# Optimization experiments

Hardware: AMD Instinct MI355X
Metric: run time of the kernel (lower is better)

The kernel has to match this reference:

```python
import jax, jax.numpy as jnp
import numpy as np
from jax import lax

B, T, H, W, C = 1, 8, 32, 32, 512


def _rmsnorm(x, gamma):
    # x / (||x||_2 + 1e-8) * sqrt(C) * gamma  (matches FlaxHunyuanVideo15RMSNorm)
    n = x / (jnp.linalg.norm(x, axis=-1, keepdims=True) + 1e-8)
    return n * (x.shape[-1] ** 0.5) * gamma


def _conv3d(x, w, b):
    # x: [B,T,H,W,Cin], w: [kt,kh,kw,Cin,Cout] (DHWIO), VALID padding
    y = lax.conv_general_dilated(x, w, (1, 1, 1), 'VALID',
                                 dimension_numbers=('NDHWC', 'DHWIO', 'NDHWC'))
    return y + b


def _causal_conv3d(x, w, b):
    # replicate pad: time (2,0) causal, spatial (1,1) each side, then valid 3x3x3 conv
    xp = jnp.pad(x, [(0, 0), (2, 0), (1, 1), (1, 1), (0, 0)], mode='edge')
    return _conv3d(xp, w, b)


def _conv1x1(x, w, b):
    # w: [1,1,1,Cin,Cout]
    return jnp.einsum('bthwc,cd->bthwd', x, w[0, 0, 0]) + b


def _resnet(x, g1, w1, b1, g2, w2, b2):
    h = jax.nn.silu(_rmsnorm(x, g1))
    h = _causal_conv3d(h, w1, b1)
    h = jax.nn.silu(_rmsnorm(h, g2))
    h = _causal_conv3d(h, w2, b2)
    return h + x


def _attn(x, g, qw, qb, kw, kb, vw, vb, pw, pb):
    identity = x
    xn = _rmsnorm(x, g)
    b, t, h, w, c = xn.shape
    n_hw = h * w
    s = t * n_hw
    q = _conv1x1(xn, qw, qb).reshape(b, s, c)
    k = _conv1x1(xn, kw, kb).reshape(b, s, c)
    v = _conv1x1(xn, vw, vb).reshape(b, s, c)
    # block-causal frame mask: query at frame f attends to keys with frame <= f
    fid = jnp.arange(s) // n_hw
    mask = jnp.where(fid[None, :] <= fid[:, None], 0.0, -jnp.inf).astype(q.dtype)
    scale = 1.0 / jnp.sqrt(jnp.asarray(c, q.dtype))
    scores = jnp.einsum('bqc,bkc->bqk', q, k) * scale + mask  # [B,S,S]
    attn = jax.nn.softmax(scores, axis=-1)
    o = jnp.einsum('bqk,bkc->bqc', attn, v).reshape(b, t, h, w, c)
    o = _conv1x1(o, pw, pb)
    return o + identity


def _forward(x, r1_g1, r1_w1, r1_b1, r1_g2, r1_w2, r1_b2,
             at_g, q_w, q_b, k_w, k_b, v_w, v_b, p_w, p_b,
             r2_g1, r2_w1, r2_b1, r2_g2, r2_w2, r2_b2):
    h = _resnet(x, r1_g1, r1_w1, r1_b1, r1_g2, r1_w2, r1_b2)
    h = _attn(h, at_g, q_w, q_b, k_w, k_b, v_w, v_b, p_w, p_b)
    h = _resnet(h, r2_g1, r2_w1, r2_b1, r2_g2, r2_w2, r2_b2)
    return h


def setup_inputs() -> dict:
    key = jax.random.key(0)
    ks = jax.random.split(key, 10)
    w3 = lambda k: jax.random.normal(k, (3, 3, 3, C, C), jnp.float32) * 0.02
    w1 = lambda k: jax.random.normal(k, (1, 1, 1, C, C), jnp.float32) * 0.02
    zc = jnp.zeros((C,), jnp.float32)
    oc = jnp.ones((C,), jnp.float32)
    return dict(
        x=jax.random.normal(ks[0], (B, T, H, W, C), jnp.float32),
        r1_g1=oc, r1_w1=w3(ks[1]), r1_b1=zc,
        r1_g2=oc, r1_w2=w3(ks[2]), r1_b2=zc,
        at_g=oc,
        q_w=w1(ks[3]), q_b=zc,
        k_w=w1(ks[4]), k_b=zc,
        v_w=w1(ks[5]), v_b=zc,
        p_w=w1(ks[6]), p_b=zc,
        r2_g1=oc, r2_w1=w3(ks[7]), r2_b1=zc,
        r2_g2=oc, r2_w2=w3(ks[8]), r2_b2=zc,
    )


def reference(x, r1_g1, r1_w1, r1_b1, r1_g2, r1_w2, r1_b2,
              at_g, q_w, q_b, k_w, k_b, v_w, v_b, p_w, p_b,
              r2_g1, r2_w1, r2_b1, r2_g2, r2_w2, r2_b2):
    return _forward(x, r1_g1, r1_w1, r1_b1, r1_g2, r1_w2, r1_b2,
                    at_g, q_w, q_b, k_w, k_b, v_w, v_b, p_w, p_b,
                    r2_g1, r2_w1, r2_b1, r2_g2, r2_w2, r2_b2)
```

## Files before the change

kernel.cpp:

```cpp
#include <hip/hip_runtime.h>
#include <cstdint>
#include <cstddef>

typedef __attribute__((ext_vector_type(4))) float floatx4;
typedef __attribute__((ext_vector_type(8))) short short8;

__device__ __forceinline__ short f2bf(float x) {
  union { float f; unsigned u; } c; c.f = x;
  unsigned r = (c.u + 0x7FFFu + ((c.u >> 16) & 1u)) >> 16;
  return (short)r;
}

__device__ __forceinline__ float bf2f(short x) {
  union { unsigned u; float f; } c; c.u = ((unsigned)(unsigned short)x) << 16;
  return c.f;
}

__device__ __forceinline__ floatx4 mfma16(short8 a, short8 b, floatx4 c) {
  return __builtin_amdgcn_mfma_f32_16x16x32_bf16(a, b, c, 0, 0, 0);
}

template <typename T>
__device__ __forceinline__ void gl_lds16(const T* g, T* l) {
  __builtin_amdgcn_global_load_lds(
      (__attribute__((address_space(1))) void*)g,
      (__attribute__((address_space(3))) void*)l, 16, 0, 0);
}

template <bool PAD, bool SILU>
__global__ __launch_bounds__(256) void norm_kernel(const float* __restrict__ src,
                                                   const float* __restrict__ gamma,
                                                   short* __restrict__ dst) {
  const int tid = threadIdx.x;
  const int wv = tid >> 6, lane = tid & 63;
  const int id = blockIdx.x * 4 + wv;
  int srow;
  if (PAD) {
    int tp = id / 1156, rem = id - tp * 1156;
    int hp = rem / 34, wp = rem - hp * 34;
    int t = tp - 2; t = t < 0 ? 0 : t;
    int h = hp - 1; h = h < 0 ? 0 : (h > 31 ? 31 : h);
    int w = wp - 1; w = w < 0 ? 0 : (w > 31 ? 31 : w);
    srow = (t << 10) + (h << 5) + w;
  } else {
    srow = id;
  }
  const float* sp = src + (size_t)srow * 512 + lane * 8;
  float4 v0 = *(const float4*)sp;
  float4 v1 = *(const float4*)(sp + 4);
  float a[8] = {v0.x, v0.y, v0.z, v0.w, v1.x, v1.y, v1.z, v1.w};
  float ss = 0.f;
#pragma unroll
  for (int i = 0; i < 8; ++i) ss += a[i] * a[i];
#pragma unroll
  for (int off = 32; off > 0; off >>= 1) ss += __shfl_xor(ss, off);
  const float scale = 22.627416997969522f / (sqrtf(ss) + 1e-8f);
  const float* gp = gamma + lane * 8;
  float4 g0 = *(const float4*)gp;
  float4 g1 = *(const float4*)(gp + 4);
  float g[8] = {g0.x, g0.y, g0.z, g0.w, g1.x, g1.y, g1.z, g1.w};
  short8 ov;
#pragma unroll
  for (int i = 0; i < 8; ++i) {
    float y = a[i] * scale * g[i];
    if (SILU) y = y / (1.f + __expf(-y));
    ov[i] = f2bf(y);
  }
  *(short8*)(dst + (size_t)id * 512 + lane * 8) = ov;
}

__global__ __launch_bounds__(256) void combine_norm(const float* __restrict__ P0,
                                                    const float* __restrict__ P1,
                                                    const float* __restrict__ bias,
                                                    const float* __restrict__ gamma,
                                                    short* __restrict__ dst) {
  const int tid = threadIdx.x;
  const int wv = tid >> 6, lane = tid & 63;
  const int id = blockIdx.x * 4 + wv;
  int tp = id / 1156, rem = id - tp * 1156;
  int hp = rem / 34, wp = rem - hp * 34;
  int t = tp - 2; t = t < 0 ? 0 : t;
  int h = hp - 1; h = h < 0 ? 0 : (h > 31 ? 31 : h);
  int w = wp - 1; w = w < 0 ? 0 : (w > 31 ? 31 : w);
  const int srow = (t << 10) + (h << 5) + w;
  const float* sp0 = P0 + (size_t)srow * 512 + lane * 8;
  const float* sp1 = P1 + (size_t)srow * 512 + lane * 8;
  float4 a0 = *(const float4*)sp0, a1 = *(const float4*)(sp0 + 4);
  float4 b0 = *(const float4*)sp1, b1 = *(const float4*)(sp1 + 4);
  float4 z0 = *(const float4*)(bias + lane * 8), z1 = *(const float4*)(bias + lane * 8 + 4);
  float a[8] = {a0.x + b0.x + z0.x, a0.y + b0.y + z0.y, a0.z + b0.z + z0.z, a0.w + b0.w + z0.w,
                a1.x + b1.x + z1.x, a1.y + b1.y + z1.y, a1.z + b1.z + z1.z, a1.w + b1.w + z1.w};
  float ss = 0.f;
#pragma unroll
  for (int i = 0; i < 8; ++i) ss += a[i] * a[i];
#pragma unroll
  for (int off = 32; off > 0; off >>= 1) ss += __shfl_xor(ss, off);
  const float scale = 22.627416997969522f / (sqrtf(ss) + 1e-8f);
  float4 g0 = *(const float4*)(gamma + lane * 8), g1 = *(const float4*)(gamma + lane * 8 + 4);
  float g[8] = {g0.x, g0.y, g0.z, g0.w, g1.x, g1.y, g1.z, g1.w};
  short8 ov;
#pragma unroll
  for (int i = 0; i < 8; ++i) {
    float y = a[i] * scale * g[i];
    y = y / (1.f + __expf(-y));
    ov[i] = f2bf(y);
  }
  *(short8*)(dst + (size_t)id * 512 + lane * 8) = ov;
}

__global__ __launch_bounds__(256) void transpose_w(const float* __restrict__ src,
                                                   short* __restrict__ dst, int R, int C) {
  __shared__ float t[32][33];
  const int tx = threadIdx.x & 31, ty = threadIdx.x >> 5;
  const int r0 = (int)blockIdx.x << 5, c0 = (int)blockIdx.y << 5;
#pragma unroll
  for (int i = 0; i < 4; ++i)
    t[ty + i * 8][tx] = src[(size_t)(r0 + ty + i * 8) * C + c0 + tx];
  __syncthreads();
#pragma unroll
  for (int i = 0; i < 4; ++i)
    dst[(size_t)(c0 + ty + i * 8) * R + r0 + tx] = f2bf(t[tx][ty + i * 8]);
}

__global__ __launch_bounds__(256) void conv_gemm_sp(const short* __restrict__ Xp,
                                                    const short* __restrict__ WT,
                                                    float* __restrict__ P0,
                                                    float* __restrict__ P1) {
  __shared__ __attribute__((aligned(16))) short Alds[2][4096];
  __shared__ __attribute__((aligned(16))) short Blds[2][4096];
  const int tid = threadIdx.x;
  const int wv = tid >> 6, lane = tid & 63;
  const int m0 = (int)blockIdx.x << 7, n0 = (int)blockIdx.y << 7;
  const int z = blockIdx.z;
  float* __restrict__ dst = z ? P1 : P0;

  int aoff[2], boff[2];
#pragma unroll
  for (int j = 0; j < 2; ++j) {
    const int chunk = wv * 2 + j;
    const int m = m0 + chunk * 16 + (lane >> 2);
    const int t = m >> 10, h = (m >> 5) & 31, w = m & 31;
    aoff[j] = (t * 1156 + h * 34 + w) * 512 + (lane & 3) * 8;
    const int n = n0 + chunk * 16 + (lane >> 2);
    boff[j] = n * 13824 + (lane & 3) * 8;
  }
  const int wm = (wv & 1) << 6, wn = (wv >> 1) << 6;
  floatx4 acc[4][4];
#pragma unroll
  for (int i = 0; i < 4; ++i)
#pragma unroll
    for (int j = 0; j < 4; ++j) acc[i][j] = 0.f;

  const int la = (lane & 15) * 32 + (lane >> 4) * 8;
  const int k0 = z * 216, k1 = k0 + 216;

  auto stage = [&](int kk, int buf) {
    const int tap = kk >> 4;
    const int cin0 = (kk & 15) << 5;
    const int dt = tap / 9;
    const int r9 = tap - dt * 9;
    const int dh = r9 / 3;
    const int dw = r9 - dh * 3;
    const int tapoff = (dt * 1156 + dh * 34 + dw) * 512 + cin0;
#pragma unroll
    for (int j = 0; j < 2; ++j) {
      const int chunk = wv * 2 + j;
      gl_lds16(Xp + aoff[j] + tapoff, &Alds[buf][chunk * 512]);
      gl_lds16(WT + boff[j] + (kk << 5), &Blds[buf][chunk * 512]);
    }
  };

  stage(k0, 0);
  for (int kk = k0; kk < k1; ++kk) {
    const int cur = (kk - k0) & 1;
    __syncthreads();
    if (kk + 1 < k1) stage(kk + 1, cur ^ 1);
    short8 af[4], bf[4];
#pragma unroll
    for (int i = 0; i < 4; ++i) af[i] = *(const short8*)&Alds[cur][(wm + i * 16) * 32 + la];
#pragma unroll
    for (int j = 0; j < 4; ++j) bf[j] = *(const short8*)&Blds[cur][(wn + j * 16) * 32 + la];
#pragma unroll
    for (int i = 0; i < 4; ++i)
#pragma unroll
      for (int j = 0; j < 4; ++j) acc[i][j] = mfma16(af[i], bf[j], acc[i][j]);
  }

  const int rbase = m0 + wm + (lane >> 4) * 4;
#pragma unroll
  for (int i = 0; i < 4; ++i) {
    const int row = rbase + i * 16;
#pragma unroll
    for (int j = 0; j < 4; ++j) {
      const int col = n0 + wn + j * 16 + (lane & 15);
#pragma unroll
      for (int r = 0; r < 4; ++r)
        dst[(size_t)(row + r) * 512 + col] = acc[i][j][r];
    }
  }
}

template <bool HAS_RES>
__global__ __launch_bounds__(256) void conv_combine(const float* __restrict__ P0,
                                                    const float* __restrict__ P1,
                                                    const float* __restrict__ bias,
                                                    const float* __restrict__ res,
                                                    float* __restrict__ out) {
  const size_t i = ((size_t)blockIdx.x * 256 + threadIdx.x) * 4;
  float4 a = *(const float4*)(P0 + i);
  float4 b = *(const float4*)(P1 + i);
  float4 bz = *(const float4*)(bias + (int)(i & 511));
  float4 r;
  r.x = a.x + b.x + bz.x;
  r.y = a.y + b.y + bz.y;
  r.z = a.z + b.z + bz.z;
  r.w = a.w + b.w + bz.w;
  if (HAS_RES) {
    float4 rs = *(const float4*)(res + i);
    r.x += rs.x; r.y += rs.y; r.z += rs.z; r.w += rs.w;
  }
  *(float4*)(out + i) = r;
}

template <int EPI>
__global__ __launch_bounds__(256) void gemm_bt(const short* __restrict__ A,
                                               const short* __restrict__ BT, int kdim,
                                               const float* __restrict__ b0,
                                               const float* __restrict__ b1,
                                               const float* __restrict__ b2,
                                               short* __restrict__ o0,
                                               short* __restrict__ o1,
                                               short* __restrict__ o2,
                                               float* oF, const float* res) {
  __shared__ __attribute__((aligned(16))) short Alds[2][4096];
  __shared__ __attribute__((aligned(16))) short Blds[2][4096];
  const int tid = threadIdx.x;
  const int wv = tid >> 6, lane = tid & 63;
  const int m0 = (int)blockIdx.x << 7, n0 = (int)blockIdx.y << 7;
  int aoff[2], boff[2];
#pragma unroll
  for (int j = 0; j < 2; ++j) {
    const int chunk = wv * 2 + j;
    aoff[j] = (m0 + chunk * 16 + (lane >> 2)) * kdim + (lane & 3) * 8;
    boff[j] = (n0 + chunk * 16 + (lane >> 2)) * kdim + (lane & 3) * 8;
  }
  const int wm = (wv & 1) << 6, wn = (wv >> 1) << 6;
  floatx4 acc[4][4];
#pragma unroll
  for (int i = 0; i < 4; ++i)
#pragma unroll
    for (int j = 0; j < 4; ++j) acc[i][j] = 0.f;
  const int la = (lane & 15) * 32 + (lane >> 4) * 8;
  const int kiters = kdim >> 5;

  auto stage = [&](int kk, int buf) {
#pragma unroll
    for (int j = 0; j < 2; ++j) {
      const int chunk = wv * 2 + j;
      gl_lds16(A + aoff[j] + (kk << 5), &Alds[buf][chunk * 512]);
      gl_lds16(BT + boff[j] + (kk << 5), &Blds[buf][chunk * 512]);
    }
  };

  stage(0, 0);
  for (int kk = 0; kk < kiters; ++kk) {
    const int cur = kk & 1;
    __syncthreads();
    if (kk + 1 < kiters) stage(kk + 1, cur ^ 1);
    short8 af[4], bf[4];
#pragma unroll
    for (int i = 0; i < 4; ++i) af[i] = *(const short8*)&Alds[cur][(wm + i * 16) * 32 + la];
#pragma unroll
    for (int j = 0; j < 4; ++j) bf[j] = *(const short8*)&Blds[cur][(wn + j * 16) * 32 + la];
#pragma unroll
    for (int i = 0; i < 4; ++i)
#pragma unroll
      for (int j = 0; j < 4; ++j) acc[i][j] = mfma16(af[i], bf[j], acc[i][j]);
  }

  const int rbase = m0 + wm + (lane >> 4) * 4;
#pragma unroll
  for (int i = 0; i < 4; ++i) {
    const int row = rbase + i * 16;
#pragma unroll
    for (int j = 0; j < 4; ++j) {
      const int col = n0 + wn + j * 16 + (lane & 15);
      if (EPI == 0) {
        const int sel = col >> 9;
        const int c = col & 511;
        const float* bp = sel == 0 ? b0 : (sel == 1 ? b1 : b2);
        const float bz = bp[c];
#pragma unroll
        for (int r = 0; r < 4; ++r) {
          const int rr = row + r;
          const short v = f2bf(acc[i][j][r] + bz);
          if (sel == 0) {
            o0[(size_t)rr * 512 + c] = v;
          } else if (sel == 1) {
            o1[(size_t)(rr >> 5) * 16384 + ((c >> 5) << 10) + (((c >> 3) & 3) << 8) +
               ((rr & 31) << 3) + (c & 7)] = v;
          } else {
            o2[(size_t)(rr >> 5) * 16384 + (((rr >> 3) & 3) << 12) + (c << 3) + (rr & 7)] = v;
          }
        }
      } else {
        const float bz = b0[col];
#pragma unroll
        for (int r = 0; r < 4; ++r) {
          const size_t idx = (size_t)(row + r) * 512 + col;
          oF[idx] = acc[i][j][r] + bz + res[idx];
        }
      }
    }
  }
}

__global__ __launch_bounds__(512, 2) void attn_partial(const short* __restrict__ Q,
                                                       const short* __restrict__ Ksw,
                                                       const short* __restrict__ Vsw,
                                                       short* __restrict__ OpA,
                                                       short* __restrict__ OpB,
                                                       float* __restrict__ Lp) {
  __shared__ __attribute__((aligned(16))) short Kl[2][16384];
  __shared__ __attribute__((aligned(16))) short Vl[2][16384];
  __shared__ __attribute__((aligned(16))) short Plds[8][512];
  const int tid = threadIdx.x;
  const int wv = tid >> 6, lane = tid & 63;
  const int cl = lane & 15, quad = lane >> 4;
  const int bid = (int)blockIdx.x;
  const int u = ((bid >> 5) << 3) | (bid & 7);
  const int w4 = (bid >> 3) & 3;
  const int y = u >> 1;
  const int qb = ((u & 1) << 2) | w4;
  int f = 0;
  while ((f + 1) * (f + 2) / 2 <= y) ++f;
  const int chunk = y - f * (f + 1) / 2;
  const int pidx = y * 8 + qb;
  const int q0 = (f << 10) + (qb << 7);

  short8 qf[16];
  {
    const short* qp = Q + (size_t)(q0 + wv * 16 + cl) * 512 + quad * 8;
#pragma unroll
    for (int kc = 0; kc < 16; ++kc) qf[kc] = *(const short8*)(qp + kc * 32);
  }
  floatx4 o[32];
#pragma unroll
  for (int i = 0; i < 32; ++i) o[i] = 0.f;
  float lr[4] = {0.f, 0.f, 0.f, 0.f};
  const float c1 = 0.063758716f;
  const int swr = ((cl >> 1) & 3) << 3;

  auto stage = [&](int kt, int buf) {
    const size_t tb = (size_t)((chunk << 5) + kt) * 16384;
    const short* kg = Ksw + tb + (wv << 11);
    const short* vg = Vsw + tb + (wv << 11);
    short* kl = &Kl[buf][wv << 11];
    short* vl = &Vl[buf][wv << 11];
#pragma unroll
    for (int i = 0; i < 4; ++i) {
      gl_lds16(kg + (i << 9) + lane * 8, kl + (i << 9));
      gl_lds16(vg + (i << 9) + lane * 8, vl + (i << 9));
    }
  };

  stage(0, 0);
  for (int kt = 0; kt < 32; ++kt) {
    const int cur = kt & 1;
    __syncthreads();
    if (kt + 1 < 32) stage(kt + 1, cur ^ 1);

    const short* klb = &Kl[cur][quad * 256 + cl * 8];
    floatx4 s0 = 0.f, s1 = 0.f;
#pragma unroll
    for (int kc = 0; kc < 16; ++kc) {
      short8 k0 = *(const short8*)(klb + kc * 1024);
      short8 k1 = *(const short8*)(klb + kc * 1024 + 128);
      s0 = mfma16(qf[kc], k0, s0);
      s1 = mfma16(qf[kc], k1, s1);
    }

#pragma unroll
    for (int r = 0; r < 4; ++r) {
      const float p0 = exp2f(s0[r] * c1), p1 = exp2f(s1[r] * c1);
      float ps = p0 + p1;
      ps += __shfl_xor(ps, 1);
      ps += __shfl_xor(ps, 2);
      ps += __shfl_xor(ps, 4);
      ps += __shfl_xor(ps, 8);
      lr[r] += ps;
      const int qlr = quad * 4 + r;
      const int sw = ((qlr >> 1) & 3) << 3;
      const int oi = qlr * 32 + (cl ^ sw);
      Plds[wv][oi] = f2bf(p0);
      Plds[wv][oi ^ 16] = f2bf(p1);
    }
    const short8 pf = *(const short8*)&Plds[wv][cl * 32 + ((quad << 3) ^ swr)];
    const short* vlb = &Vl[cur][quad * 4096 + cl * 8];
#pragma unroll
    for (int cn = 0; cn < 32; ++cn) {
      const short8 vf = *(const short8*)(vlb + cn * 128);
      o[cn] = mfma16(pf, vf, o[cn]);
    }
  }

  short* base = pidx < 108 ? OpA + (size_t)pidx * 65536 : OpB + (size_t)(pidx - 108) * 65536;
  const int lrow0 = wv * 16 + quad * 4;
#pragma unroll
  for (int cn = 0; cn < 32; ++cn) {
    const int col = cn * 16 + cl;
#pragma unroll
    for (int r = 0; r < 4; ++r)
      base[(size_t)(lrow0 + r) * 512 + col] = f2bf(o[cn][r]);
  }
  if (cl == 0) {
#pragma unroll
    for (int r = 0; r < 4; ++r) Lp[pidx * 128 + lrow0 + r] = lr[r];
  }
}

__global__ __launch_bounds__(256) void attn_combine(const short* __restrict__ OpA,
                                                    const short* __restrict__ OpB,
                                                    const float* __restrict__ Lp,
                                                    short* __restrict__ O) {
  const int tid = threadIdx.x;
  const int wv = tid >> 6, lane = tid & 63;
  const int row = (int)blockIdx.x * 4 + wv;
  const int f = row >> 10, n = f + 1;
  const int qb = (row >> 7) & 7, lrow = row & 127;
  const int tri = f * (f + 1) / 2;
  float den = 0.f, acc[8];
#pragma unroll
  for (int i = 0; i < 8; ++i) acc[i] = 0.f;
#pragma unroll
  for (int ch = 0; ch < 8; ++ch) {
    if (ch < n) {
      const int pidx = (tri + ch) * 8 + qb;
      den += Lp[pidx * 128 + lrow];
      const short* b = pidx < 108 ? OpA + (size_t)pidx * 65536 : OpB + (size_t)(pidx - 108) * 65536;
      const short8 v = *(const short8*)(b + (size_t)lrow * 512 + lane * 8);
#pragma unroll
      for (int i = 0; i < 8; ++i) acc[i] += bf2f(v[i]);
    }
  }
  const float inv = 1.f / den;
  short8 ov;
#pragma unroll
  for (int i = 0; i < 8; ++i) ov[i] = f2bf(acc[i] * inv);
  *(short8*)(O + (size_t)row * 512 + lane * 8) = ov;
}

extern "C" void kernel_launch(void* const* d_in, const int* in_sizes, int n_in,
                              void* d_out, int out_size, void* d_ws, size_t ws_size,
                              hipStream_t stream) {
  const float* x     = (const float*)d_in[0];
  const float* r1_g1 = (const float*)d_in[1];
  const float* r1_w1 = (const float*)d_in[2];
  const float* r1_b1 = (const float*)d_in[3];
  const float* r1_g2 = (const float*)d_in[4];
  const float* r1_w2 = (const float*)d_in[5];
  const float* r1_b2 = (const float*)d_in[6];
  const float* at_g  = (const float*)d_in[7];
  const float* q_w   = (const float*)d_in[8];
  const float* q_b   = (const float*)d_in[9];
  const float* k_w   = (const float*)d_in[10];
  const float* k_b   = (const float*)d_in[11];
  const float* v_w   = (const float*)d_in[12];
  const float* v_b   = (const float*)d_in[13];
  const float* p_w   = (const float*)d_in[14];
  const float* p_b   = (const float*)d_in[15];
  const float* r2_g1 = (const float*)d_in[16];
  const float* r2_w1 = (const float*)d_in[17];
  const float* r2_b1 = (const float*)d_in[18];
  const float* r2_g2 = (const float*)d_in[19];
  const float* r2_w2 = (const float*)d_in[20];
  const float* r2_b2 = (const float*)d_in[21];
  float* out = (float*)d_out;

  char* ws = (char*)d_ws;
  size_t off = 0;
  auto alloc = [&](size_t bytes) -> void* {
    void* p = ws + off;
    off = (off + bytes + 255) & ~(size_t)255;
    return p;
  };
  short* wT    = (short*)alloc(27ull * 512 * 512 * 2);
  short* wqkvT = (short*)alloc(1536ull * 512 * 2);
  short* pwT   = (short*)alloc(512ull * 512 * 2);
  short* Xp    = (short*)alloc(10ull * 34 * 34 * 512 * 2);
  float* Y     = (float*)alloc(8192ull * 512 * 4);
  float* hA    = (float*)alloc(8192ull * 512 * 4);
  short* xn    = (short*)alloc(8192ull * 512 * 2);
  short* Qb    = (short*)alloc(8192ull * 512 * 2);
  short* Ksw   = (short*)alloc(8192ull * 512 * 2);
  short* Vsw   = (short*)alloc(8192ull * 512 * 2);
  float* Lp    = (float*)alloc(288ull * 128 * 4);
  (void)ws_size; (void)in_sizes; (void)n_in; (void)out_size; (void)Y;

  short* OpA = wT;
  short* OpB = Xp;
  float* P0  = (float*)xn;
  float* P1  = (float*)Ksw;

  const dim3 b256(256), b512(512);
  const dim3 convg(64, 4, 2);

  transpose_w<<<dim3(432, 16), b256, 0, stream>>>(r1_w1, wT, 13824, 512);
  norm_kernel<true, true><<<2890, b256, 0, stream>>>(x, r1_g1, Xp);
  conv_gemm_sp<<<convg, b256, 0, stream>>>(Xp, wT, P0, P1);
  transpose_w<<<dim3(432, 16), b256, 0, stream>>>(r1_w2, wT, 13824, 512);
  combine_norm<<<2890, b256, 0, stream>>>(P0, P1, r1_b1, r1_g2, Xp);
  conv_gemm_sp<<<convg, b256, 0, stream>>>(Xp, wT, P0, P1);
  conv_combine<true><<<4096, b256, 0, stream>>>(P0, P1, r1_b2, x, hA);

  norm_kernel<false, false><<<2048, b256, 0, stream>>>(hA, at_g, xn);
  transpose_w<<<dim3(16, 16), b256, 0, stream>>>(q_w, wqkvT, 512, 512);
  transpose_w<<<dim3(16, 16), b256, 0, stream>>>(k_w, wqkvT + 512 * 512, 512, 512);
  transpose_w<<<dim3(16, 16), b256, 0, stream>>>(v_w, wqkvT + 1024 * 512, 512, 512);
  transpose_w<<<dim3(16, 16), b256, 0, stream>>>(p_w, pwT, 512, 512);
  gemm_bt<0><<<dim3(64, 12), b256, 0, stream>>>(xn, wqkvT, 512, q_b, k_b, v_b,
                                                Qb, Ksw, Vsw, nullptr, nullptr);
  attn_partial<<<288, b512, 0, stream>>>(Qb, Ksw, Vsw, OpA, OpB, Lp);
  attn_combine<<<2048, b256, 0, stream>>>(OpA, OpB, Lp, xn);
  gemm_bt<1><<<dim3(64, 4), b256, 0, stream>>>(xn, pwT, 512, p_b, nullptr, nullptr,
                                               nullptr, nullptr, nullptr, hA, hA);

  transpose_w<<<dim3(432, 16), b256, 0, stream>>>(r2_w1, wT, 13824, 512);
  norm_kernel<true, true><<<2890, b256, 0, stream>>>(hA, r2_g1, Xp);
  conv_gemm_sp<<<convg, b256, 0, stream>>>(Xp, wT, P0, P1);
  transpose_w<<<dim3(432, 16), b256, 0, stream>>>(r2_w2, wT, 13824, 512);
  combine_norm<<<2890, b256, 0, stream>>>(P0, P1, r2_b1, r2_g2, Xp);
  conv_gemm_sp<<<convg, b256, 0, stream>>>(Xp, wT, P0, P1);
  conv_combine<true><<<4096, b256, 0, stream>>>(P0, P1, r2_b2, hA, out);
}
```

Baseline: 1.126 ms.

## Split first resnet convs three ways along K and shrink attention tiles to 64 rows

The first resnet's conv GEMMs now split K three ways (grid z=3) instead of two, which adds a third fp32 partial buffer that the combine kernels sum. The intent is more blocks in flight across the CUs, at the cost of extra partial-sum traffic. The attention partial kernel moves from 512-thread blocks with 128 query rows to 256-thread blocks with 64 rows, doubling the block count to 576. It also drops K/V double buffering in favour of a single buffer with two barriers per tile, and moves the row-sum shuffle reduction out of the inner loop. The second resnet keeps the two-way split, so the uneven treatment looks experimental.

New measurement: 1.068 ms. 5.1% less time.

```diff
diff --git a/kernel.cpp b/kernel.cpp
--- a/kernel.cpp
+++ b/kernel.cpp
@@ -69,8 +69,10 @@
   *(short8*)(dst + (size_t)id * 512 + lane * 8) = ov;
 }
 
+template <int NP>
 __global__ __launch_bounds__(256) void combine_norm(const float* __restrict__ P0,
                                                     const float* __restrict__ P1,
+                                                    const float* __restrict__ P2,
                                                     const float* __restrict__ bias,
                                                     const float* __restrict__ gamma,
                                                     short* __restrict__ dst) {
@@ -82,14 +84,22 @@
   int t = tp - 2; t = t < 0 ? 0 : t;
   int h = hp - 1; h = h < 0 ? 0 : (h > 31 ? 31 : h);
   int w = wp - 1; w = w < 0 ? 0 : (w > 31 ? 31 : w);
-  const int srow = (t << 10) + (h << 5) + w;
-  const float* sp0 = P0 + (size_t)srow * 512 + lane * 8;
-  const float* sp1 = P1 + (size_t)srow * 512 + lane * 8;
-  float4 a0 = *(const float4*)sp0, a1 = *(const float4*)(sp0 + 4);
-  float4 b0 = *(const float4*)sp1, b1 = *(const float4*)(sp1 + 4);
-  float4 z0 = *(const float4*)(bias + lane * 8), z1 = *(const float4*)(bias + lane * 8 + 4);
-  float a[8] = {a0.x + b0.x + z0.x, a0.y + b0.y + z0.y, a0.z + b0.z + z0.z, a0.w + b0.w + z0.w,
-                a1.x + b1.x + z1.x, a1.y + b1.y + z1.y, a1.z + b1.z + z1.z, a1.w + b1.w + z1.w};
+  const size_t base = (size_t)((t << 10) + (h << 5) + w) * 512 + lane * 8;
+  float a[8];
+  {
+    float4 a0 = *(const float4*)(P0 + base), a1 = *(const float4*)(P0 + base + 4);
+    float4 b0 = *(const float4*)(P1 + base), b1 = *(const float4*)(P1 + base + 4);
+    float4 z0 = *(const float4*)(bias + lane * 8), z1 = *(const float4*)(bias + lane * 8 + 4);
+    a[0] = a0.x + b0.x + z0.x; a[1] = a0.y + b0.y + z0.y;
+    a[2] = a0.z + b0.z + z0.z; a[3] = a0.w + b0.w + z0.w;
+    a[4] = a1.x + b1.x + z1.x; a[5] = a1.y + b1.y + z1.y;
+    a[6] = a1.z + b1.z + z1.z; a[7] = a1.w + b1.w + z1.w;
+    if (NP == 3) {
+      float4 c0 = *(const float4*)(P2 + base), c1 = *(const float4*)(P2 + base + 4);
+      a[0] += c0.x; a[1] += c0.y; a[2] += c0.z; a[3] += c0.w;
+      a[4] += c1.x; a[5] += c1.y; a[6] += c1.z; a[7] += c1.w;
+    }
+  }
   float ss = 0.f;
 #pragma unroll
   for (int i = 0; i < 8; ++i) ss += a[i] * a[i];
@@ -122,17 +132,20 @@
     dst[(size_t)(c0 + ty + i * 8) * R + r0 + tx] = f2bf(t[tx][ty + i * 8]);
 }
 
+template <int NP>
 __global__ __launch_bounds__(256) void conv_gemm_sp(const short* __restrict__ Xp,
                                                     const short* __restrict__ WT,
                                                     float* __restrict__ P0,
-                                                    float* __restrict__ P1) {
+                                                    float* __restrict__ P1,
+                                                    float* __restrict__ P2) {
   __shared__ __attribute__((aligned(16))) short Alds[2][4096];
   __shared__ __attribute__((aligned(16))) short Blds[2][4096];
   const int tid = threadIdx.x;
   const int wv = tid >> 6, lane = tid & 63;
   const int m0 = (int)blockIdx.x << 7, n0 = (int)blockIdx.y << 7;
   const int z = blockIdx.z;
-  float* __restrict__ dst = z ? P1 : P0;
+  float* __restrict__ dst = (NP == 3) ? (z == 0 ? P0 : (z == 1 ? P1 : P2))
+                                      : (z ? P1 : P0);
 
   int aoff[2], boff[2];
 #pragma unroll
@@ -152,7 +165,8 @@
     for (int j = 0; j < 4; ++j) acc[i][j] = 0.f;
 
   const int la = (lane & 15) * 32 + (lane >> 4) * 8;
-  const int k0 = z * 216, k1 = k0 + 216;
+  const int span = 432 / NP;
+  const int k0 = z * span, k1 = k0 + span;
 
   auto stage = [&](int kk, int buf) {
     const int tap = kk >> 4;
@@ -200,9 +214,10 @@
   }
 }
 
-template <bool HAS_RES>
+template <int NP, bool HAS_RES>
 __global__ __launch_bounds__(256) void conv_combine(const float* __restrict__ P0,
                                                     const float* __restrict__ P1,
+                                                    const float* __restrict__ P2,
                                                     const float* __restrict__ bias,
                                                     const float* __restrict__ res,
                                                     float* __restrict__ out) {
@@ -215,6 +230,10 @@
   r.y = a.y + b.y + bz.y;
   r.z = a.z + b.z + bz.z;
   r.w = a.w + b.w + bz.w;
+  if (NP == 3) {
+    float4 c = *(const float4*)(P2 + i);
+    r.x += c.x; r.y += c.y; r.z += c.z; r.w += c.w;
+  }
   if (HAS_RES) {
     float4 rs = *(const float4*)(res + i);
     r.x += rs.x; r.y += rs.y; r.z += rs.z; r.w += rs.w;
@@ -315,28 +334,34 @@
   }
 }
 
-__global__ __launch_bounds__(512, 2) void attn_partial(const short* __restrict__ Q,
+__global__ __launch_bounds__(256, 2) void attn_partial(const short* __restrict__ Q,
                                                        const short* __restrict__ Ksw,
                                                        const short* __restrict__ Vsw,
                                                        short* __restrict__ OpA,
                                                        short* __restrict__ OpB,
                                                        float* __restrict__ Lp) {
-  __shared__ __attribute__((aligned(16))) short Kl[2][16384];
-  __shared__ __attribute__((aligned(16))) short Vl[2][16384];
-  __shared__ __attribute__((aligned(16))) short Plds[8][512];
+  __shared__ __attribute__((aligned(16))) short Klds[16384];
+  __shared__ __attribute__((aligned(16))) short Vlds[16384];
+  __shared__ __attribute__((aligned(16))) short Plds[4][512];
   const int tid = threadIdx.x;
   const int wv = tid >> 6, lane = tid & 63;
   const int cl = lane & 15, quad = lane >> 4;
   const int bid = (int)blockIdx.x;
-  const int u = ((bid >> 5) << 3) | (bid & 7);
-  const int w4 = (bid >> 3) & 3;
-  const int y = u >> 1;
-  const int qb = ((u & 1) << 2) | w4;
+  const int x8 = bid & 7, jj = bid >> 3;
+  int y, qb;
+  if (jj < 64) {
+    y = x8 + ((jj >> 4) << 3);
+    qb = jj & 15;
+  } else {
+    const int L = x8 * 8 + (jj - 64);
+    y = 32 + (L >> 4);
+    qb = L & 15;
+  }
   int f = 0;
   while ((f + 1) * (f + 2) / 2 <= y) ++f;
   const int chunk = y - f * (f + 1) / 2;
-  const int pidx = y * 8 + qb;
-  const int q0 = (f << 10) + (qb << 7);
+  const int pidx = y * 16 + qb;
+  const int q0 = (f << 10) + (qb << 6);
 
   short8 qf[16];
   {
@@ -349,28 +374,20 @@
   for (int i = 0; i < 32; ++i) o[i] = 0.f;
   float lr[4] = {0.f, 0.f, 0.f, 0.f};
   const float c1 = 0.063758716f;
+  const short* klb = Klds + quad * 256 + cl * 8;
+  const short* vlb = Vlds + quad * 4096 + cl * 8;
   const int swr = ((cl >> 1) & 3) << 3;
 
-  auto stage = [&](int kt, int buf) {
+  for (int kt = 0; kt < 32; ++kt) {
     const size_t tb = (size_t)((chunk << 5) + kt) * 16384;
-    const short* kg = Ksw + tb + (wv << 11);
-    const short* vg = Vsw + tb + (wv << 11);
-    short* kl = &Kl[buf][wv << 11];
-    short* vl = &Vl[buf][wv << 11];
-#pragma unroll
-    for (int i = 0; i < 4; ++i) {
-      gl_lds16(kg + (i << 9) + lane * 8, kl + (i << 9));
-      gl_lds16(vg + (i << 9) + lane * 8, vl + (i << 9));
-    }
-  };
-
-  stage(0, 0);
-  for (int kt = 0; kt < 32; ++kt) {
-    const int cur = kt & 1;
+#pragma unroll
+    for (int j = 0; j < 8; ++j) {
+      const int row = (j * 4 + wv) << 9;
+      gl_lds16(Ksw + tb + row + lane * 8, &Klds[row]);
+      gl_lds16(Vsw + tb + row + lane * 8, &Vlds[row]);
+    }
     __syncthreads();
-    if (kt + 1 < 32) stage(kt + 1, cur ^ 1);
-
-    const short* klb = &Kl[cur][quad * 256 + cl * 8];
+
     floatx4 s0 = 0.f, s1 = 0.f;
 #pragma unroll
     for (int kc = 0; kc < 16; ++kc) {
@@ -383,12 +400,7 @@
 #pragma unroll
     for (int r = 0; r < 4; ++r) {
       const float p0 = exp2f(s0[r] * c1), p1 = exp2f(s1[r] * c1);
-      float ps = p0 + p1;
-      ps += __shfl_xor(ps, 1);
-      ps += __shfl_xor(ps, 2);
-      ps += __shfl_xor(ps, 4);
-      ps += __shfl_xor(ps, 8);
-      lr[r] += ps;
+      lr[r] += p0 + p1;
       const int qlr = quad * 4 + r;
       const int sw = ((qlr >> 1) & 3) << 3;
       const int oi = qlr * 32 + (cl ^ sw);
@@ -396,15 +408,25 @@
       Plds[wv][oi ^ 16] = f2bf(p1);
     }
     const short8 pf = *(const short8*)&Plds[wv][cl * 32 + ((quad << 3) ^ swr)];
-    const short* vlb = &Vl[cur][quad * 4096 + cl * 8];
 #pragma unroll
     for (int cn = 0; cn < 32; ++cn) {
       const short8 vf = *(const short8*)(vlb + cn * 128);
       o[cn] = mfma16(pf, vf, o[cn]);
     }
-  }
-
-  short* base = pidx < 108 ? OpA + (size_t)pidx * 65536 : OpB + (size_t)(pidx - 108) * 65536;
+    __syncthreads();
+  }
+
+#pragma unroll
+  for (int r = 0; r < 4; ++r) {
+    float v = lr[r];
+    v += __shfl_xor(v, 1);
+    v += __shfl_xor(v, 2);
+    v += __shfl_xor(v, 4);
+    v += __shfl_xor(v, 8);
+    lr[r] = v;
+  }
+
+  short* base = pidx < 216 ? OpA + (size_t)pidx * 32768 : OpB + (size_t)(pidx - 216) * 32768;
   const int lrow0 = wv * 16 + quad * 4;
 #pragma unroll
   for (int cn = 0; cn < 32; ++cn) {
@@ -415,7 +437,7 @@
   }
   if (cl == 0) {
 #pragma unroll
-    for (int r = 0; r < 4; ++r) Lp[pidx * 128 + lrow0 + r] = lr[r];
+    for (int r = 0; r < 4; ++r) Lp[pidx * 64 + lrow0 + r] = lr[r];
   }
 }
 
@@ -427,7 +449,7 @@
   const int wv = tid >> 6, lane = tid & 63;
   const int row = (int)blockIdx.x * 4 + wv;
   const int f = row >> 10, n = f + 1;
-  const int qb = (row >> 7) & 7, lrow = row & 127;
+  const int qb = (row >> 6) & 15, lrow = row & 63;
   const int tri = f * (f + 1) / 2;
   float den = 0.f, acc[8];
 #pragma unroll
@@ -435,9 +457,9 @@
 #pragma unroll
   for (int ch = 0; ch < 8; ++ch) {
     if (ch < n) {
-      const int pidx = (tri + ch) * 8 + qb;
-      den += Lp[pidx * 128 + lrow];
-      const short* b = pidx < 108 ? OpA + (size_t)pidx * 65536 : OpB + (size_t)(pidx - 108) * 65536;
+      const int pidx = (tri + ch) * 16 + qb;
+      den += Lp[pidx * 64 + lrow];
+      const short* b = pidx < 216 ? OpA + (size_t)pidx * 32768 : OpB + (size_t)(pidx - 216) * 32768;
       const short8 v = *(const short8*)(b + (size_t)lrow * 512 + lane * 8);
 #pragma unroll
       for (int i = 0; i < 8; ++i) acc[i] += bf2f(v[i]);
@@ -494,24 +516,26 @@
   short* Qb    = (short*)alloc(8192ull * 512 * 2);
   short* Ksw   = (short*)alloc(8192ull * 512 * 2);
   short* Vsw   = (short*)alloc(8192ull * 512 * 2);
-  float* Lp    = (float*)alloc(288ull * 128 * 4);
-  (void)ws_size; (void)in_sizes; (void)n_in; (void)out_size; (void)Y;
+  float* Lp    = (float*)alloc(576ull * 64 * 4);
+  (void)ws_size; (void)in_sizes; (void)n_in; (void)out_size;
 
   short* OpA = wT;
   short* OpB = Xp;
   float* P0  = (float*)xn;
   float* P1  = (float*)Ksw;
-
-  const dim3 b256(256), b512(512);
-  const dim3 convg(64, 4, 2);
+  float* P2  = Y;
+
+  const dim3 b256(256);
+  const dim3 convg3(64, 4, 3);
+  const dim3 convg2(64, 4, 2);
 
   transpose_w<<<dim3(432, 16), b256, 0, stream>>>(r1_w1, wT, 13824, 512);
   norm_kernel<true, true><<<2890, b256, 0, stream>>>(x, r1_g1, Xp);
-  conv_gemm_sp<<<convg, b256, 0, stream>>>(Xp, wT, P0, P1);
+  conv_gemm_sp<3><<<convg3, b256, 0, stream>>>(Xp, wT, P0, P1, P2);
   transpose_w<<<dim3(432, 16), b256, 0, stream>>>(r1_w2, wT, 13824, 512);
-  combine_norm<<<2890, b256, 0, stream>>>(P0, P1, r1_b1, r1_g2, Xp);
-  conv_gemm_sp<<<convg, b256, 0, stream>>>(Xp, wT, P0, P1);
-  conv_combine<true><<<4096, b256, 0, stream>>>(P0, P1, r1_b2, x, hA);
+  combine_norm<3><<<2890, b256, 0, stream>>>(P0, P1, P2, r1_b1, r1_g2, Xp);
+  conv_gemm_sp<3><<<convg3, b256, 0, stream>>>(Xp, wT, P0, P1, P2);
+  conv_combine<3, true><<<4096, b256, 0, stream>>>(P0, P1, P2, r1_b2, x, hA);
 
   norm_kernel<false, false><<<2048, b256, 0, stream>>>(hA, at_g, xn);
   transpose_w<<<dim3(16, 16), b256, 0, stream>>>(q_w, wqkvT, 512, 512);
@@ -520,16 +544,16 @@
   transpose_w<<<dim3(16, 16), b256, 0, stream>>>(p_w, pwT, 512, 512);
   gemm_bt<0><<<dim3(64, 12), b256, 0, stream>>>(xn, wqkvT, 512, q_b, k_b, v_b,
                                                 Qb, Ksw, Vsw, nullptr, nullptr);
-  attn_partial<<<288, b512, 0, stream>>>(Qb, Ksw, Vsw, OpA, OpB, Lp);
+  attn_partial<<<576, b256, 0, stream>>>(Qb, Ksw, Vsw, OpA, OpB, Lp);
   attn_combine<<<2048, b256, 0, stream>>>(OpA, OpB, Lp, xn);
   gemm_bt<1><<<dim3(64, 4), b256, 0, stream>>>(xn, pwT, 512, p_b, nullptr, nullptr,
                                                nullptr, nullptr, nullptr, hA, hA);
 
   transpose_w<<<dim3(432, 16), b256, 0, stream>>>(r2_w1, wT, 13824, 512);
   norm_kernel<true, true><<<2890, b256, 0, stream>>>(hA, r2_g1, Xp);
-  conv_gemm_sp<<<convg, b256, 0, stream>>>(Xp, wT, P0, P1);
+  conv_gemm_sp<2><<<convg2, b256, 0, stream>>>(Xp, wT, P0, P1, P2);
   transpose_w<<<dim3(432, 16), b256, 0, stream>>>(r2_w2, wT, 13824, 512);
-  combine_norm<<<2890, b256, 0, stream>>>(P0, P1, r2_b1, r2_g2, Xp);
-  conv_gemm_sp<<<convg, b256, 0, stream>>>(Xp, wT, P0, P1);
-  conv_combine<true><<<4096, b256, 0, stream>>>(P0, P1, r2_b2, hA, out);
-}
+  combine_norm<2><<<2890, b256, 0, stream>>>(P0, P1, P2, r2_b1, r2_g2, Xp);
+  conv_gemm_sp<2><<<convg2, b256, 0, stream>>>(Xp, wT, P0, P1, P2);
+  conv_combine<2, true><<<4096, b256, 0, stream>>>(P0, P1, P2, r2_b2, hA, out);
+}
```
